# Kernel optimization log

Hardware: AMD Instinct MI355X
Metric: run time of the kernel (lower is better)

## Reference

```python
import jax, jax.numpy as jnp
import numpy as np
import math

EMBED_DIM = 768
NUM_HEADS = 12
SEQ_LEN = 2048
NUM_BLOCKS = 8
BLOCK_SIZE = EMBED_DIM // NUM_BLOCKS  # 96
HEAD_DIM = EMBED_DIM // NUM_HEADS     # 64
BATCH = 4


def build_sparse_mask(T):
    # local window of 5 (j in [i-4, i]) plus log-stride links at i-8, i-16, ...
    m = np.full((T, T), -np.inf, dtype=np.float32)
    for i in range(T):
        for j in range(max(0, i - 4), i + 1):
            m[i, j] = 0.0
        step = 8
        while i - step >= 0:
            m[i, i - step] = 0.0
            step *= 2
    return jnp.asarray(m)


def make_urdhva_params(key):
    k1, k2, k3 = jax.random.split(key, 3)
    s = BLOCK_SIZE ** 0.5
    Wv = jax.random.normal(k1, (NUM_BLOCKS, BLOCK_SIZE, BLOCK_SIZE), jnp.float32) / s
    Wr = jax.random.normal(k2, (NUM_BLOCKS - 1, BLOCK_SIZE, BLOCK_SIZE), jnp.float32) / s
    Wl = jax.random.normal(k3, (NUM_BLOCKS - 1, BLOCK_SIZE, BLOCK_SIZE), jnp.float32) / s
    b = jnp.zeros((EMBED_DIM,), jnp.float32)
    return Wv, Wr, Wl, b


def urdhva_linear(x, Wv, Wr, Wl, b):
    # x: [..., EMBED_DIM] -> block-diagonal + neighbor cross-block linear
    shp = x.shape
    xb = x.reshape(-1, NUM_BLOCKS, BLOCK_SIZE)  # [N, B, S]
    y = jnp.einsum('nbs,bst->nbt', xb, Wv)
    y = y.at[:, 1:, :].add(jnp.einsum('nbs,bst->nbt', xb[:, :-1, :], Wr))
    y = y.at[:, :-1, :].add(jnp.einsum('nbs,bst->nbt', xb[:, 1:, :], Wl))
    return y.reshape(shp) + b


def setup_inputs() -> dict:
    key = jax.random.key(0)
    kx, kq, kk, kv, ko = jax.random.split(key, 5)
    inp = {'x': jax.random.normal(kx, (BATCH, SEQ_LEN, EMBED_DIM), jnp.float32)}
    for name, k in (('q', kq), ('k', kk), ('v', kv), ('o', ko)):
        Wv, Wr, Wl, b = make_urdhva_params(k)
        inp[name + '_Wv'] = Wv
        inp[name + '_Wr'] = Wr
        inp[name + '_Wl'] = Wl
        inp[name + '_b'] = b
    inp['sparse_mask'] = build_sparse_mask(SEQ_LEN)
    return inp


def reference(x, q_Wv, q_Wr, q_Wl, q_b, k_Wv, k_Wr, k_Wl, k_b,
              v_Wv, v_Wr, v_Wl, v_b, o_Wv, o_Wr, o_Wl, o_b, sparse_mask):
    B, T, C = x.shape
    H, D = NUM_HEADS, HEAD_DIM
    q = urdhva_linear(x, q_Wv, q_Wr, q_Wl, q_b).reshape(B, T, H, D).transpose(0, 2, 1, 3)
    k = urdhva_linear(x, k_Wv, k_Wr, k_Wl, k_b).reshape(B, T, H, D).transpose(0, 2, 1, 3)
    v = urdhva_linear(x, v_Wv, v_Wr, v_Wl, v_b).reshape(B, T, H, D).transpose(0, 2, 1, 3)
    scores = jnp.einsum('bhqd,bhkd->bhqk', q, k) / math.sqrt(D)
    scores = scores + sparse_mask[:T, :T]
    attn = jax.nn.softmax(scores, axis=-1)
    out = jnp.einsum('bhqk,bhkd->bhqd', attn, v).transpose(0, 2, 1, 3).reshape(B, T, C)
    return urdhva_linear(out, o_Wv, o_Wr, o_Wl, o_b)
```

## Files before the change

kernel.cpp:

```cpp
#include <hip/hip_runtime.h>
#include <hip/hip_bf16.h>

typedef __hip_bfloat16 bf16;
typedef __attribute__((ext_vector_type(8))) short short8;
typedef __attribute__((ext_vector_type(4))) float f32x4;

#define ED 768
#define NB 8
#define BS 96
#define NH 12
#define HD 64
#define SEQ 2048
#define NBATCH 4
#define NROWS (NBATCH*SEQ)

__device__ __forceinline__ float b2f(bf16 v){ return __bfloat162float(v); }
__device__ __forceinline__ bf16 f2b(float v){ return __float2bfloat16(v); }
__device__ __forceinline__ short f2bs(float v){
    return (short)__builtin_bit_cast(unsigned short, __float2bfloat16(v));
}
__device__ __forceinline__ unsigned pkbf16(float lo, float hi){
    return (unsigned)(unsigned short)f2bs(lo) |
           ((unsigned)(unsigned short)f2bs(hi) << 16);
}
__device__ __forceinline__ void gload_lds16(const void* g, void* l) {
    __builtin_amdgcn_global_load_lds(
        (const __attribute__((address_space(1))) unsigned*)g,
        (__attribute__((address_space(3))) unsigned*)l, 16, 0, 0);
}

#define XCVT_BLKS (NROWS*ED/8/256)
#define DENS_BLKS (ED*ED/256)
__global__ __launch_bounds__(256) void prep(
    const float* __restrict__ x, bf16* __restrict__ xb,
    const float* __restrict__ qWv, const float* __restrict__ qWr, const float* __restrict__ qWl,
    const float* __restrict__ kWv, const float* __restrict__ kWr, const float* __restrict__ kWl,
    const float* __restrict__ vWv, const float* __restrict__ vWr, const float* __restrict__ vWl,
    const float* __restrict__ oWv, const float* __restrict__ oWr, const float* __restrict__ oWl,
    bf16* __restrict__ WdBase)
{
    if (blockIdx.x < XCVT_BLKS) {
        const int idx = blockIdx.x*256 + threadIdx.x;
        const float4 a = ((const float4*)x)[(size_t)idx*2];
        const float4 c = ((const float4*)x)[(size_t)idx*2 + 1];
        short8 o;
        o[0]=f2bs(a.x); o[1]=f2bs(a.y); o[2]=f2bs(a.z); o[3]=f2bs(a.w);
        o[4]=f2bs(c.x); o[5]=f2bs(c.y); o[6]=f2bs(c.z); o[7]=f2bs(c.w);
        ((short8*)xb)[idx] = o;
    } else {
        const int bid = blockIdx.x - XCVT_BLKS;
        const int z = bid / DENS_BLKS;
        const float* Wv = (z==0)?qWv:(z==1)?kWv:(z==2)?vWv:oWv;
        const float* Wr = (z==0)?qWr:(z==1)?kWr:(z==2)?vWr:oWr;
        const float* Wl = (z==0)?qWl:(z==1)?kWl:(z==2)?vWl:oWl;
        bf16* Wd = WdBase + (size_t)z*ED*ED;

        const int idx = (bid - z*DENS_BLKS)*256 + threadIdx.x;
        const int t = idx / ED, s = idx - t*ED;
        const int bt = t / BS, tt = t - bt*BS;
        const int bs = s / BS, ss = s - bs*BS;
        float val = 0.f;
        if (bs == bt)        val = Wv[(bt*BS + ss)*BS + tt];
        else if (bs == bt-1) val = Wr[((bt-1)*BS + ss)*BS + tt];
        else if (bs == bt+1) val = Wl[(bt*BS + ss)*BS + tt];
        Wd[idx] = f2b(val);
    }
}

__device__ __forceinline__ void stage64(
    const bf16* __restrict__ Ag, const bf16* __restrict__ Wd,
    int rowbase, int colbase, int k0,
    bf16* As, bf16* Bs, int wave, int lane)
{
    const int r8 = lane >> 3;
    const int sl = lane & 7;
    const int kofs = ((sl ^ r8) << 3);
    #pragma unroll
    for (int c = wave; c < 28; c += 4) {
        if (c < 16) {
            const int row = c*8 + r8;
            gload_lds16(Ag + (size_t)(rowbase + row)*ED + k0 + kofs,
                        (char*)As + c*1024);
        } else {
            const int row = (c-16)*8 + r8;
            gload_lds16(Wd + (size_t)(colbase + row)*ED + k0 + kofs,
                        (char*)Bs + (c-16)*1024);
        }
    }
}

__device__ __forceinline__ void compute64(
    const bf16* As, const bf16* Bs, int wave, int lane, f32x4 acc[2][6])
{
    const int l15 = lane & 15;
    const int s   = lane >> 4;
    #pragma unroll
    for (int ks = 0; ks < 2; ++ks) {
        short8 a[2], b[6];
        #pragma unroll
        for (int rf = 0; rf < 2; ++rf) {
            const int row = wave*32 + rf*16 + l15;
            a[rf] = *(const short8*)((const char*)As + row*128 +
                        ((((ks<<2)+s) ^ (row&7)) << 4));
        }
        #pragma unroll
        for (int nf = 0; nf < 6; ++nf) {
            const int row = nf*16 + l15;
            b[nf] = *(const short8*)((const char*)Bs + row*128 +
                        ((((ks<<2)+s) ^ (row&7)) << 4));
        }
        #pragma unroll
        for (int rf = 0; rf < 2; ++rf)
            #pragma unroll
            for (int nf = 0; nf < 6; ++nf)
                acc[rf][nf] = __builtin_amdgcn_mfma_f32_16x16x32_bf16(
                                  a[rf], b[nf], acc[rf][nf], 0, 0, 0);
    }
}

__device__ __forceinline__ void stage32(
    const bf16* __restrict__ Ag, const bf16* __restrict__ Wd,
    int rowbase, int colbase, int k0,
    bf16* As, bf16* Bs, int wave, int lane)
{
    const int sub  = lane >> 2;
    const int slot = lane & 3;
    const int sws  = ((lane >> 2) ^ (lane >> 4)) & 3;
    const int kofs = ((slot ^ sws) << 3);
    #pragma unroll
    for (int c = wave; c < 14; c += 4) {
        if (c < 8) {
            const int r = c*16 + sub;
            gload_lds16(Ag + (size_t)(rowbase + r)*ED + k0 + kofs,
                        (char*)As + c*1024);
        } else {
            const int col = (c-8)*16 + sub;
            gload_lds16(Wd + (size_t)(colbase + col)*ED + k0 + kofs,
                        (char*)Bs + (c-8)*1024);
        }
    }
}

__device__ __forceinline__ void compute32(
    const bf16* As, const bf16* Bs, int wave, int lane, f32x4 acc[2][6])
{
    const int l15 = lane & 15;
    const int s   = lane >> 4;
    const int swr = (l15 ^ (l15 >> 2)) & 3;
    const int rsel = ((s ^ swr) << 4);

    short8 a[2], b[6];
    #pragma unroll
    for (int rf = 0; rf < 2; ++rf)
        a[rf] = *(const short8*)((const char*)As +
                    (wave*32 + rf*16 + l15)*64 + rsel);
    #pragma unroll
    for (int nf = 0; nf < 6; ++nf)
        b[nf] = *(const short8*)((const char*)Bs + (nf*16 + l15)*64 + rsel);
    #pragma unroll
    for (int rf = 0; rf < 2; ++rf)
        #pragma unroll
        for (int nf = 0; nf < 6; ++nf)
            acc[rf][nf] = __builtin_amdgcn_mfma_f32_16x16x32_bf16(
                              a[rf], b[nf], acc[rf][nf], 0, 0, 0);
}

template<bool OBF16>
__global__ __launch_bounds__(256, 2) void urdhva_gemm_lds(
    const bf16* __restrict__ A,
    const bf16* __restrict__ WdBase,
    const float* __restrict__ bias0, const float* __restrict__ bias1,
    const float* __restrict__ bias2,
    void* __restrict__ OutBase)
{
    __shared__ __align__(16) bf16 As[2][128*64];
    __shared__ __align__(16) bf16 Bs[2][96*64];

    const int z = blockIdx.z;
    const bf16* Wd = WdBase + (size_t)z*ED*ED;
    const float* bias = (z==0) ? bias0 : (z==1) ? bias1 : bias2;

    const int lane = threadIdx.x & 63;
    const int wave = threadIdx.x >> 6;
    const int rowbase = blockIdx.x*128;
    const int ob = blockIdx.y;
    const int colbase = ob*BS;
    const int klo = (ob==0)    ? 0  : (ob-1)*BS;
    const int khi = (ob==NB-1) ? ED : (ob+2)*BS;
    const int band = khi - klo;
    const int nt64 = band >> 6;
    const bool tail = (band & 63) != 0;

    f32x4 acc[2][6];
    #pragma unroll
    for (int i=0;i<2;++i)
        #pragma unroll
        for (int j=0;j<6;++j) acc[i][j] = (f32x4){0.f,0.f,0.f,0.f};

    stage64(A, Wd, rowbase, colbase, klo, As[0], Bs[0], wave, lane);
    __syncthreads();
    int cur = 0;
    for (int t = 1; t < nt64; ++t) {
        stage64(A, Wd, rowbase, colbase, klo + t*64,
                As[cur^1], Bs[cur^1], wave, lane);
        compute64(As[cur], Bs[cur], wave, lane, acc);
        __syncthreads();
        cur ^= 1;
    }
    if (tail) {
        stage32(A, Wd, rowbase, colbase, klo + nt64*64,
                As[cur^1], Bs[cur^1], wave, lane);
        compute64(As[cur], Bs[cur], wave, lane, acc);
        __syncthreads();
        cur ^= 1;
        compute32(As[cur], Bs[cur], wave, lane, acc);
    } else {
        compute64(As[cur], Bs[cur], wave, lane, acc);
    }

    const int l15 = lane & 15;
    const int rbase = (lane >> 4) * 4;
    const int wrow = rowbase + wave*32;
    if (OBF16 && z == 2) {
        bf16* vT = (bf16*)OutBase + (size_t)2*NROWS*ED;
        #pragma unroll
        for (int rf = 0; rf < 2; ++rf) {
            #pragma unroll
            for (int nf = 0; nf < 6; ++nf) {
                const int col = colbase + nf*16 + l15;
                const float bv = bias[col];
                const int row0 = wrow + rf*16 + rbase;
                uint2 dw;
                dw.x = pkbf16(acc[rf][nf][0] + bv, acc[rf][nf][1] + bv);
                dw.y = pkbf16(acc[rf][nf][2] + bv, acc[rf][nf][3] + bv);
                *(uint2*)(vT + ((size_t)(row0 >> 4)*ED + col)*16 + (row0 & 15)) = dw;
            }
        }
    } else {
        #pragma unroll
        for (int rf = 0; rf < 2; ++rf) {
            #pragma unroll
            for (int nf = 0; nf < 6; ++nf) {
                const int col = colbase + nf*16 + l15;
                const float bv = bias[col];
                #pragma unroll
                for (int r = 0; r < 4; ++r) {
                    const int row = wrow + rf*16 + rbase + r;
                    const float vv = acc[rf][nf][r] + bv;
                    if (OBF16)
                        ((bf16*)OutBase)[(size_t)z*NROWS*ED + (size_t)row*ED + col] = f2b(vv);
                    else
                        ((float*)OutBase)[(size_t)row*ED + col] = vv;
                }
            }
        }
    }
}

__global__ __launch_bounds__(256) void sparse_attn_mfma(
    const bf16* __restrict__ q, const bf16* __restrict__ k,
    const bf16* __restrict__ vT, bf16* __restrict__ out)
{
    __shared__ __align__(16) unsigned short Plds[4][16][136];

    const int lane = threadIdx.x & 63;
    const int wid  = threadIdx.x >> 6;
    const int o  = (blockIdx.x & 7)*192 + (blockIdx.x >> 3);
    const int w  = o*4 + wid;
    const int qt = w & 127;
    const int hb = w >> 7;
    const int h  = hb % NH;
    const int bb = hb / NH;
    const int i0 = qt << 4;

    const int l15 = lane & 15;
    const int g   = lane >> 4;

    const bf16* qbase = q + ((size_t)bb*SEQ + i0 + l15)*ED + h*HD + g*8;
    const short8 qf0 = *(const short8*)qbase;
    const short8 qf1 = *(const short8*)(qbase + 32);

    int bases[8];
    bases[0]=i0;     bases[1]=i0-16;  bases[2]=i0-32;  bases[3]=i0-64;
    bases[4]=i0-128; bases[5]=i0-256; bases[6]=i0-512; bases[7]=i0-1024;

    short8 vfrag[4][4];
    #pragma unroll
    for (int u = 0; u < 4; ++u) {
        const int tb = (g & 2) ? bases[2*u+1] : bases[2*u];
        const size_t gt = (size_t)bb*128 + ((tb < 0 ? 0 : tb) >> 4);
        #pragma unroll
        for (int nt = 0; nt < 4; ++nt)
            vfrag[u][nt] = *(const short8*)(vT +
                (gt*ED + h*HD + 16*nt + l15)*16 + 8*(g & 1));
    }

    const bf16* kbb = k + (size_t)bb*SEQ*ED + h*HD;

    float p[8][4];
    #pragma unroll
    for (int t = 0; t < 8; ++t) {
        f32x4 acc = (f32x4){0.f,0.f,0.f,0.f};
        if (bases[t] >= 0) {
            const bf16* kp = kbb + (size_t)(bases[t] + l15)*ED + g*8;
            const short8 kf0 = *(const short8*)kp;
            const short8 kf1 = *(const short8*)(kp + 32);
            acc = __builtin_amdgcn_mfma_f32_16x16x32_bf16(kf0, qf0, acc, 0,0,0);
            acc = __builtin_amdgcn_mfma_f32_16x16x32_bf16(kf1, qf1, acc, 0,0,0);
        }
        const int Dt = i0 - bases[t];
        #pragma unroll
        for (int r = 0; r < 4; ++r) {
            const int delta = Dt + l15 - 4*g - r;
            const bool val = (bases[t] >= 0) &&
                (((unsigned)delta <= 4u) ||
                 (delta >= 8 && (delta & (delta-1)) == 0));
            p[t][r] = val ? acc[r]*0.125f : -1e30f;
        }
    }

    float m = -1e30f;
    #pragma unroll
    for (int t = 0; t < 8; ++t)
        #pragma unroll
        for (int r = 0; r < 4; ++r) m = fmaxf(m, p[t][r]);
    m = fmaxf(m, __shfl_xor(m, 16));
    m = fmaxf(m, __shfl_xor(m, 32));

    float den = 0.f;
    #pragma unroll
    for (int t = 0; t < 8; ++t)
        #pragma unroll
        for (int r = 0; r < 4; ++r) { p[t][r] = __expf(p[t][r] - m); den += p[t][r]; }
    den += __shfl_xor(den, 16);
    den += __shfl_xor(den, 32);
    const float inv = 1.f / den;

    {
        char* prow = (char*)&Plds[wid][l15][0];
        #pragma unroll
        for (int t = 0; t < 8; ++t) {
            *(unsigned*)(prow + 32*t + 8*g)     = pkbf16(p[t][0]*inv, p[t][1]*inv);
            *(unsigned*)(prow + 32*t + 8*g + 4) = pkbf16(p[t][2]*inv, p[t][3]*inv);
        }
    }

    f32x4 accO[4];
    #pragma unroll
    for (int nt = 0; nt < 4; ++nt) accO[nt] = (f32x4){0.f,0.f,0.f,0.f};

    #pragma unroll
    for (int u = 0; u < 4; ++u) {
        const short8 pa = *(const short8*)((char*)&Plds[wid][l15][0] + 64*u + 16*g);
        #pragma unroll
        for (int nt = 0; nt < 4; ++nt)
            accO[nt] = __builtin_amdgcn_mfma_f32_16x16x32_bf16(
                           pa, vfrag[u][nt], accO[nt], 0,0,0);
    }

    #pragma unroll
    for (int nt = 0; nt < 4; ++nt)
        #pragma unroll
        for (int r = 0; r < 4; ++r)
            out[((size_t)bb*SEQ + i0 + 4*g + r)*ED + h*HD + 16*nt + l15] =
                f2b(accO[nt][r]);
}

extern "C" void kernel_launch(void* const* d_in, const int* in_sizes, int n_in,
                              void* d_out, int out_size, void* d_ws, size_t ws_size,
                              hipStream_t stream) {
    const float* x   = (const float*)d_in[0];
    const float* qWv = (const float*)d_in[1];
    const float* qWr = (const float*)d_in[2];
    const float* qWl = (const float*)d_in[3];
    const float* qb  = (const float*)d_in[4];
    const float* kWv = (const float*)d_in[5];
    const float* kWr = (const float*)d_in[6];
    const float* kWl = (const float*)d_in[7];
    const float* kb  = (const float*)d_in[8];
    const float* vWv = (const float*)d_in[9];
    const float* vWr = (const float*)d_in[10];
    const float* vWl = (const float*)d_in[11];
    const float* vb  = (const float*)d_in[12];
    const float* oWv = (const float*)d_in[13];
    const float* oWr = (const float*)d_in[14];
    const float* oWl = (const float*)d_in[15];
    const float* ob  = (const float*)d_in[16];

    const size_t QKV = (size_t)NROWS*ED;
    bf16* xb  = (bf16*)d_ws;
    bf16* q   = xb + QKV;
    bf16* k   = q + QKV;
    bf16* vT  = k + QKV;
    bf16* ao  = vT + QKV;
    bf16* Wd  = ao + QKV;
    bf16* Wdo = Wd + (size_t)3*ED*ED;

    prep<<<XCVT_BLKS + 4*DENS_BLKS, 256, 0, stream>>>(
        x, xb,
        qWv,qWr,qWl, kWv,kWr,kWl, vWv,vWr,vWl, oWv,oWr,oWl, Wd);

    urdhva_gemm_lds<true><<<dim3(NROWS/128, NB, 3), 256, 0, stream>>>(
        xb, Wd, qb, kb, vb, q);

    sparse_attn_mfma<<<(NBATCH*NH*(SEQ/16))/4, 256, 0, stream>>>(q, k, vT, ao);

    urdhva_gemm_lds<false><<<dim3(NROWS/128, NB, 1), 256, 0, stream>>>(
        ao, Wdo, ob, ob, ob, d_out);
}
```

Baseline: 71.87 us.

## Stage shared K tiles in LDS for four consecutive query tiles per block

```diff
diff --git a/kernel.cpp b/kernel.cpp
--- a/kernel.cpp
+++ b/kernel.cpp
@@ -261,17 +261,17 @@
     const bf16* __restrict__ q, const bf16* __restrict__ k,
     const bf16* __restrict__ vT, bf16* __restrict__ out)
 {
-    __shared__ __align__(16) unsigned short Plds[4][16][136];
+    __shared__ __align__(16) char shm[24*16*128];
 
     const int lane = threadIdx.x & 63;
     const int wid  = threadIdx.x >> 6;
-    const int o  = (blockIdx.x & 7)*192 + (blockIdx.x >> 3);
-    const int w  = o*4 + wid;
-    const int qt = w & 127;
-    const int hb = w >> 7;
-    const int h  = hb % NH;
-    const int bb = hb / NH;
-    const int i0 = qt << 4;
+    const int o   = (blockIdx.x & 7)*192 + (blockIdx.x >> 3);
+    const int hb  = o >> 5;
+    const int qt0 = (o & 31) << 2;
+    const int h   = hb % NH;
+    const int bb  = hb / NH;
+    const int I   = qt0 << 4;
+    const int i0  = I + (wid << 4);
 
     const int l15 = lane & 15;
     const int g   = lane >> 4;
@@ -296,15 +296,32 @@
     }
 
     const bf16* kbb = k + (size_t)bb*SEQ*ED + h*HD;
+    #pragma unroll
+    for (int c = 0; c < 12; ++c) {
+        const int id  = c*256 + threadIdx.x;
+        const int row = id >> 3;
+        const int sl  = id & 7;
+        const int j   = row >> 4;
+        int tb;
+        if (j < 8) tb = I + 48 - (j << 4);
+        else       tb = I + (((j-8) >> 2) << 4) - (128 << ((j-8) & 3));
+        const int gr = (tb < 0 ? 0 : tb) + (row & 15);
+        gload_lds16(kbb + (size_t)gr*ED + ((sl ^ (row & 7)) << 3),
+                    shm + id*16);
+    }
+    __syncthreads();
 
     float p[8][4];
     #pragma unroll
     for (int t = 0; t < 8; ++t) {
+        const int j = (t < 4) ? ((t == 3 ? 7 : 3 + t) - wid)
+                              : (8 + 4*wid + (t - 4));
         f32x4 acc = (f32x4){0.f,0.f,0.f,0.f};
         if (bases[t] >= 0) {
-            const bf16* kp = kbb + (size_t)(bases[t] + l15)*ED + g*8;
-            const short8 kf0 = *(const short8*)kp;
-            const short8 kf1 = *(const short8*)(kp + 32);
+            const char* kr = shm + (j*16 + l15)*128;
+            const int sw = l15 & 7;
+            const short8 kf0 = *(const short8*)(kr + ((g ^ sw) << 4));
+            const short8 kf1 = *(const short8*)(kr + (((g+4) ^ sw) << 4));
             acc = __builtin_amdgcn_mfma_f32_16x16x32_bf16(kf0, qf0, acc, 0,0,0);
             acc = __builtin_amdgcn_mfma_f32_16x16x32_bf16(kf1, qf1, acc, 0,0,0);
         }
@@ -336,8 +353,10 @@
     den += __shfl_xor(den, 32);
     const float inv = 1.f / den;
 
+    __syncthreads();
+
     {
-        char* prow = (char*)&Plds[wid][l15][0];
+        char* prow = shm + wid*4352 + l15*272;
         #pragma unroll
         for (int t = 0; t < 8; ++t) {
             *(unsigned*)(prow + 32*t + 8*g)     = pkbf16(p[t][0]*inv, p[t][1]*inv);
@@ -351,7 +370,7 @@
 
     #pragma unroll
     for (int u = 0; u < 4; ++u) {
-        const short8 pa = *(const short8*)((char*)&Plds[wid][l15][0] + 64*u + 16*g);
+        const short8 pa = *(const short8*)(shm + wid*4352 + l15*272 + 64*u + 16*g);
         #pragma unroll
         for (int nt = 0; nt < 4; ++nt)
             accO[nt] = __builtin_amdgcn_mfma_f32_16x16x32_bf16(
```

Measured after the change: 68.04 us. 1.06x faster.
